# Kernel tuning notes

Hardware: AMD Instinct MI355X
Metric: run time of the kernel (lower is better)

The kernel has to match this reference:

```python
import jax, jax.numpy as jnp
import numpy as np

B, TGT, SRC, DIM = 8, 1024, 1024, 1024

def setup_inputs() -> dict:
    key = jax.random.key(0)
    k1, k2, k3, k4, k5 = jax.random.split(key, 5)
    s = 1.0 / np.sqrt(DIM)
    return {
        "input": jax.random.normal(k1, (B, TGT, DIM), dtype=jnp.float32),
        "context": jax.random.normal(k2, (B, SRC, DIM), dtype=jnp.float32),
        "context_lengths": jax.random.randint(k3, (B,), 1, SRC + 1, dtype=jnp.int64 if jax.config.jax_enable_x64 else jnp.int32),
        "W_in": jax.random.normal(k4, (DIM, DIM), dtype=jnp.float32) * s,   # torch Linear weight [out,in]
        "W_out": jax.random.normal(k5, (DIM, 2 * DIM), dtype=jnp.float32) * s,
    }

def reference(input, context, context_lengths, W_in, W_out):
    # GlobalAttention, attn_type='general', include_rnn=True, dropout=0 (identity)
    # score: (W_in @ h_t) . h_s  -> [B, TGT, SRC]
    h_t = jnp.einsum('btd,ed->bte', input, W_in)
    align = jnp.einsum('bte,bse->bts', h_t, context)
    # mask positions >= length with -inf before softmax over source dim
    mask = jnp.arange(align.shape[-1])[None, :] < context_lengths[:, None]  # [B, SRC]
    align = jnp.where(mask[:, None, :], align, -jnp.inf)
    align_vectors = jax.nn.softmax(align, axis=-1)                         # [B, TGT, SRC]
    c = jnp.einsum('bts,bsd->btd', align_vectors, context)                 # context vector
    concat = jnp.concatenate([c, input], axis=-1)                          # [B, TGT, 2*DIM]
    attn_h = jnp.tanh(jnp.einsum('btf,df->btd', concat, W_out))            # linear_out (no bias) + tanh
    return attn_h, align_vectors
```

## Files before the change

kernel.cpp:

```cpp
#include <hip/hip_runtime.h>

typedef __attribute__((ext_vector_type(8))) short short8;
typedef __attribute__((ext_vector_type(4))) float f32x4;

#define DIM  1024
#define BT   8192
#define NBAT 8

__device__ __forceinline__ unsigned short f2bf(float x){
  union { float f; unsigned u; } un; un.f = x;
  unsigned r = un.u + 0x7fffu + ((un.u >> 16) & 1u);
  return (unsigned short)(r >> 16);
}
__device__ __forceinline__ float bf2f(unsigned short h){
  union { unsigned u; float f; } un; un.u = ((unsigned)h) << 16;
  return un.f;
}

__global__ void split_kernel(const float* __restrict__ x,
                             unsigned short* __restrict__ hi,
                             unsigned short* __restrict__ lo,
                             int n4){
  int stride = gridDim.x * blockDim.x;
  for (int i = blockIdx.x * blockDim.x + threadIdx.x; i < n4; i += stride){
    float4 v = ((const float4*)x)[i];
    ushort4 h, l;
    h.x = f2bf(v.x); l.x = f2bf(v.x - bf2f(h.x));
    h.y = f2bf(v.y); l.y = f2bf(v.y - bf2f(h.y));
    h.z = f2bf(v.z); l.z = f2bf(v.z - bf2f(h.z));
    h.w = f2bf(v.w); l.w = f2bf(v.w - bf2f(h.w));
    ((ushort4*)hi)[i] = h;
    ((ushort4*)lo)[i] = l;
  }
}

__global__ void cvt_kernel(const float* __restrict__ x,
                           unsigned short* __restrict__ hi, int n4){
  int stride = gridDim.x * blockDim.x;
  for (int i = blockIdx.x * blockDim.x + threadIdx.x; i < n4; i += stride){
    float4 v = ((const float4*)x)[i];
    ushort4 h;
    h.x = f2bf(v.x); h.y = f2bf(v.y); h.z = f2bf(v.z); h.w = f2bf(v.w);
    ((ushort4*)hi)[i] = h;
  }
}

__global__ void ctx_prep_kernel(const float* __restrict__ ctx,
                                unsigned short* __restrict__ hi,
                                unsigned short* __restrict__ lo,
                                unsigned short* __restrict__ ctxT){
  __shared__ unsigned short t[64][65];
  int bz = blockIdx.z;
  int s0 = blockIdx.x << 6, d0 = blockIdx.y << 6;
  int tx = threadIdx.x, ty = threadIdx.y;
  const size_t base = (((size_t)bz << 10) + s0) * DIM + d0;
  const float* src = ctx + base;
  unsigned short* hrow = hi + base;
  unsigned short* lrow = lo + base;
  #pragma unroll
  for (int i = ty; i < 64; i += 4){
    float v = src[(size_t)i * DIM + tx];
    unsigned short h = f2bf(v);
    hrow[(size_t)i * DIM + tx] = h;
    lrow[(size_t)i * DIM + tx] = f2bf(v - bf2f(h));
    t[i][tx] = h;
  }
  __syncthreads();
  unsigned short* dst = ctxT + (((size_t)bz << 10) + d0) * DIM + s0;
  #pragma unroll
  for (int i = ty; i < 64; i += 4)
    dst[(size_t)i * DIM + tx] = t[tx][i];
}

__global__ __launch_bounds__(256) void softmax_kernel(float* __restrict__ sc,
                                                      unsigned short* __restrict__ Pb,
                                                      const int* __restrict__ lens){
  const int row = blockIdx.x;
  const int len = lens[row >> 10];
  const int tid = threadIdx.x;
  const int lane = tid & 63, wid = tid >> 6;
  float* rp = sc + ((size_t)row << 10);
  const int s0 = tid << 2;
  float4 v;
  if (s0 < len) v = ((const float4*)rp)[tid];
  else          v = (float4){0.f, 0.f, 0.f, 0.f};
  float x0 = (s0 + 0 < len) ? v.x : -INFINITY;
  float x1 = (s0 + 1 < len) ? v.y : -INFINITY;
  float x2 = (s0 + 2 < len) ? v.z : -INFINITY;
  float x3 = (s0 + 3 < len) ? v.w : -INFINITY;
  float wmax = fmaxf(fmaxf(x0, x1), fmaxf(x2, x3));
  #pragma unroll
  for (int o = 32; o > 0; o >>= 1) wmax = fmaxf(wmax, __shfl_xor(wmax, o));
  __shared__ float red[8];
  if (lane == 0) red[wid] = wmax;
  __syncthreads();
  float mx = fmaxf(fmaxf(red[0], red[1]), fmaxf(red[2], red[3]));
  float e0 = (s0 + 0 < len) ? __expf(x0 - mx) : 0.f;
  float e1 = (s0 + 1 < len) ? __expf(x1 - mx) : 0.f;
  float e2 = (s0 + 2 < len) ? __expf(x2 - mx) : 0.f;
  float e3 = (s0 + 3 < len) ? __expf(x3 - mx) : 0.f;
  float ws = e0 + e1 + e2 + e3;
  #pragma unroll
  for (int o = 32; o > 0; o >>= 1) ws += __shfl_xor(ws, o);
  if (lane == 0) red[4 + wid] = ws;
  __syncthreads();
  float inv = 1.f / (red[4] + red[5] + red[6] + red[7]);
  float4 p; p.x = e0 * inv; p.y = e1 * inv; p.z = e2 * inv; p.w = e3 * inv;
  ((float4*)rp)[tid] = p;
  ushort4 pb; pb.x = f2bf(p.x); pb.y = f2bf(p.y); pb.z = f2bf(p.z); pb.w = f2bf(p.w);
  ((ushort4*)(Pb + ((size_t)row << 10)))[tid] = pb;
}

__device__ __forceinline__ int lds_off(int r, int kb){
  return r * 64 + (((kb ^ ((r >> 1) & 3))) << 4);
}

#define TILEA 16384
#define TILEB 8192

__device__ __forceinline__ void gld16(void* lds, const void* g){
  __builtin_amdgcn_global_load_lds(
      (__attribute__((address_space(1))) void*)(g),
      (__attribute__((address_space(3))) void*)(lds), 16, 0, 0);
}

template<int EPI, int NT, int KSPLIT, int SM>
__global__ __launch_bounds__(512, 2) void gemm_pipe_kernel(
    const unsigned short* __restrict__ Ah,  const unsigned short* __restrict__ Al,
    const unsigned short* __restrict__ Ah2, const unsigned short* __restrict__ Al2,
    const unsigned short* __restrict__ Bh,  const unsigned short* __restrict__ Bl,
    int lda, int ldb,
    float* __restrict__ outF, unsigned short* __restrict__ o1,
    unsigned short* __restrict__ o2, int ldo)
{
  constexpr int OFF_AL = TILEA;
  constexpr int OFF_BH = (SM == 0) ? 2 * TILEA : TILEA;
  constexpr int OFF_BL = OFF_BH + TILEB;
  constexpr int BUFSZ_T = (SM == 2) ? (OFF_BH + TILEB) : (OFF_BL + TILEB);

  __shared__ __align__(16) char sm0[BUFSZ_T];
  __shared__ __align__(16) char sm1[BUFSZ_T];
  __shared__ __align__(16) char sm2[BUFSZ_T];

  const int tid  = threadIdx.x;
  const int lane = tid & 63;
  const int w    = tid >> 6;

  int bx = blockIdx.x, by = blockIdx.y;
  {
    int o = bx + (by << 3);
    int xcd = o & 7, j = o >> 3;
    bx = j & 7;
    by = xcd * (gridDim.y >> 3) + (j >> 3);
  }
  const int m0 = by << 8;
  const int n0 = bx << 7;

  const unsigned short* gAh  = Ah  + (size_t)m0 * lda;
  const unsigned short* gAl  = Al  + (size_t)m0 * lda;
  const unsigned short* gAh2 = Ah2 + (size_t)m0 * lda;
  const unsigned short* gAl2 = Al2 + (size_t)m0 * lda;
  const unsigned short* gBh  = Bh  + (size_t)n0 * ldb;
  const unsigned short* gBl  = Bl  + (size_t)n0 * ldb;

  const int rA0 = (w << 5) + (lane >> 2);
  const int rA1 = rA0 + 16;
  const int rB0 = (w << 4) + (lane >> 2);
  const int cA0 = ((lane & 3) ^ ((rA0 >> 1) & 3)) << 3;
  const int cA1 = ((lane & 3) ^ ((rA1 >> 1) & 3)) << 3;
  const int cB0 = ((lane & 3) ^ ((rB0 >> 1) & 3)) << 3;
  const unsigned short* pAh0  = gAh  + (size_t)rA0 * lda + cA0;
  const unsigned short* pAh1  = gAh  + (size_t)rA1 * lda + cA1;
  const unsigned short* pAl0  = gAl  + (size_t)rA0 * lda + cA0;
  const unsigned short* pAl1  = gAl  + (size_t)rA1 * lda + cA1;
  const unsigned short* pAh20 = gAh2 + (size_t)rA0 * lda + cA0;
  const unsigned short* pAh21 = gAh2 + (size_t)rA1 * lda + cA1;
  const unsigned short* pAl20 = gAl2 + (size_t)rA0 * lda + cA0;
  const unsigned short* pAl21 = gAl2 + (size_t)rA1 * lda + cA1;
  const unsigned short* pBh0  = gBh  + (size_t)rB0 * ldb + cB0;
  const unsigned short* pBl0  = gBl  + (size_t)rB0 * ldb + cB0;
  const int dA0 = (w << 5) << 6;
  const int dA1 = dA0 + (16 << 6);
  const int dB0 = (w << 4) << 6;

  f32x4 acc[4][4];
  #pragma unroll
  for (int m = 0; m < 4; m++)
    #pragma unroll
    for (int n = 0; n < 4; n++)
      acc[m][n] = (f32x4){0.f, 0.f, 0.f, 0.f};

  const int wr = (w >> 1) << 6;
  const int wc = (w & 1) << 6;
  const int fr = lane & 15;
  const int kb = lane >> 4;

  short8 ah, al, bh[4], bl[4];

#define STAGE(WR, KS) do { int _k = (KS);                                   \
    const unsigned short *_s0, *_s1;                                        \
    if (KSPLIT < NT * 32 && _k >= KSPLIT){                                  \
      int _q = _k - KSPLIT;                                                 \
      _s0 = pAh20 + _q; _s1 = pAh21 + _q;                                   \
    } else { _s0 = pAh0 + _k; _s1 = pAh1 + _k; }                            \
    gld16(WR + dA0, _s0);                                                   \
    gld16(WR + dA1, _s1);                                                   \
    if constexpr (SM == 0){                                                 \
      const unsigned short *_s2, *_s3;                                      \
      if (KSPLIT < NT * 32 && _k >= KSPLIT){                                \
        int _q = _k - KSPLIT;                                               \
        _s2 = pAl20 + _q; _s3 = pAl21 + _q;                                 \
      } else { _s2 = pAl0 + _k; _s3 = pAl1 + _k; }                          \
      gld16(WR + OFF_AL + dA0, _s2);                                        \
      gld16(WR + OFF_AL + dA1, _s3);                                        \
    }                                                                       \
    gld16(WR + OFF_BH + dB0, pBh0 + _k);                                    \
    if constexpr (SM != 2)                                                  \
      gld16(WR + OFF_BL + dB0, pBl0 + _k);                                  \
  } while(0)

#define READS_B(RD) do {                                                    \
    _Pragma("unroll")                                                       \
    for (int n = 0; n < 4; n++){                                            \
      int off = lds_off(wc + n * 16 + fr, kb);                              \
      bh[n] = *(const short8*)((RD) + OFF_BH + off);                        \
      if constexpr (SM != 2)                                                \
        bl[n] = *(const short8*)((RD) + OFF_BL + off);                      \
    }                                                                       \
  } while(0)

#define READS_A(RD, M) do {                                                 \
    int off = lds_off(wr + (M) * 16 + fr, kb);                              \
    ah = *(const short8*)((RD) + off);                                      \
    if constexpr (SM == 0) al = *(const short8*)((RD) + OFF_AL + off);      \
  } while(0)

#define MFMA_M(M) do {                                                      \
    __builtin_amdgcn_s_setprio(1);                                          \
    _Pragma("unroll")                                                       \
    for (int n = 0; n < 4; n++){                                            \
      acc[M][n] = __builtin_amdgcn_mfma_f32_16x16x32_bf16(ah, bh[n], acc[M][n], 0, 0, 0); \
      if constexpr (SM != 2)                                                \
        acc[M][n] = __builtin_amdgcn_mfma_f32_16x16x32_bf16(ah, bl[n], acc[M][n], 0, 0, 0); \
      if constexpr (SM == 0)                                                \
        acc[M][n] = __builtin_amdgcn_mfma_f32_16x16x32_bf16(al, bh[n], acc[M][n], 0, 0, 0); \
    }                                                                       \
    __builtin_amdgcn_s_setprio(0);                                          \
  } while(0)

#define BAR() do { __builtin_amdgcn_s_barrier();                            \
                   asm volatile("" ::: "memory"); } while(0)
#define LGKM0() asm volatile("s_waitcnt lgkmcnt(0)" ::: "memory")
#define VMCNT_STEP() do {                                                   \
    if constexpr (SM == 0)      asm volatile("s_waitcnt vmcnt(6)" ::: "memory"); \
    else if constexpr (SM == 1) asm volatile("s_waitcnt vmcnt(4)" ::: "memory"); \
    else                        asm volatile("s_waitcnt vmcnt(3)" ::: "memory"); \
  } while(0)

#define STEP(RD, WR, T) do {                                                \
    int _ks = (((T) + 2 < NT) ? (T) + 2 : NT - 1) << 5;   \
    READS_B(RD); READS_A(RD, 0);                                            \
    STAGE(WR, _ks);                                                         \
    BAR(); LGKM0(); MFMA_M(0); BAR();                                       \
    READS_A(RD, 1);                                                        \
    BAR(); LGKM0(); MFMA_M(1); BAR();                                       \
    READS_A(RD, 2);                                                        \
    BAR(); LGKM0(); MFMA_M(2); BAR();                                       \
    READS_A(RD, 3);                                                        \
    BAR(); LGKM0(); MFMA_M(3);                                              \
    VMCNT_STEP();                                                           \
    BAR();                                                                  \
  } while(0)

  STAGE(sm0, 0);
  STAGE(sm1, 32);
  VMCNT_STEP();
  BAR();

  for (int t = 0; t < NT; t += 3){
    STEP(sm0, sm2, t);
    if (t + 1 < NT) STEP(sm1, sm0, t + 1);
    if (t + 2 < NT) STEP(sm2, sm1, t + 2);
  }
#undef STAGE
#undef READS_B
#undef READS_A
#undef MFMA_M
#undef BAR
#undef LGKM0
#undef VMCNT_STEP
#undef STEP

  const int rbase = (lane >> 4) << 2;
  const int cbase = lane & 15;
  #pragma unroll
  for (int m = 0; m < 4; m++){
    #pragma unroll
    for (int n = 0; n < 4; n++){
      f32x4 v = acc[m][n];
      int col = n0 + wc + n * 16 + cbase;
      #pragma unroll
      for (int j = 0; j < 4; j++){
        int row = m0 + wr + m * 16 + rbase + j;
        float val = v[j];
        size_t idx = (size_t)row * ldo + col;
        if (EPI == 0){
          unsigned short h = f2bf(val);
          o1[idx] = h;
          o2[idx] = f2bf(val - bf2f(h));
        } else {
          outF[idx] = tanhf(val);
        }
      }
    }
  }
}

template<bool SPLIT, int EPI>
__global__ __launch_bounds__(256, 2) void gemm_kernel(
    const unsigned short* __restrict__ Ah, const unsigned short* __restrict__ Al,
    const unsigned short* __restrict__ Bh, const unsigned short* __restrict__ Bl,
    int K, int lda, int ldb,
    long long aStride, long long bStride, long long oStride,
    float* __restrict__ outF, unsigned short* __restrict__ o1,
    unsigned short* __restrict__ o2, int ldo,
    const int* __restrict__ lens, int lmode)
{
  constexpr int TILE = 128 * 64;
  __shared__ char smem[(SPLIT ? 4 : 2) * TILE];
  char* sAh = smem;
  char* sBh = smem + TILE;
  char* sAl = smem + (SPLIT ? 2 : 0) * TILE;
  char* sBl = smem + (SPLIT ? 3 : 0) * TILE;

  const int tid  = threadIdx.x;
  const int lane = tid & 63;
  const int wid  = tid >> 6;
  const int z    = blockIdx.z;

  int bx = blockIdx.x, by = blockIdx.y;
  if (gridDim.x == 8 && gridDim.y == 8){
    int o = bx + (by << 3);
    int k = o & 7, j = o >> 3;
    bx = ((k & 3) << 1) | (j & 1);  by = ((k >> 2) << 2) | (j >> 1);
  }
  const int m0 = by * 128;
  const int n0 = bx * 128;

  int Keff = K;
  if (lmode){
    const int len = lens[z];
    if (lmode == 1 && n0 >= len) return;
    if (lmode == 2){
      int kc = (len + 31) & ~31;
      Keff = kc < K ? kc : K;
    }
  }

  const unsigned short* gAh = Ah + (size_t)z * aStride + (size_t)m0 * lda;
  const unsigned short* gBh = Bh + (size_t)z * bStride + (size_t)n0 * ldb;
  const unsigned short* gAl = SPLIT ? (Al + (size_t)z * aStride + (size_t)m0 * lda) : (const unsigned short*)0;
  const unsigned short* gBl = SPLIT ? (Bl + (size_t)z * bStride + (size_t)n0 * ldb) : (const unsigned short*)0;

  f32x4 acc[4][4];
  #pragma unroll
  for (int m = 0; m < 4; m++)
    #pragma unroll
    for (int n = 0; n < 4; n++)
      acc[m][n] = (f32x4){0.f, 0.f, 0.f, 0.f};

  const int wr = (wid >> 1) * 64;
  const int wc = (wid & 1) * 64;
  const int fr = lane & 15;
  const int kb = lane >> 4;

  for (int k0 = 0; k0 < Keff; k0 += 32){
    __syncthreads();
    #pragma unroll
    for (int it = 0; it < 2; ++it){
      int c = tid + it * 256;
      int r = c >> 2, kk = c & 3;
      int lo = lds_off(r, kk);
      size_t ga = (size_t)r * lda + k0 + kk * 8;
      size_t gb = (size_t)r * ldb + k0 + kk * 8;
      *(short8*)(sAh + lo) = *(const short8*)(gAh + ga);
      *(short8*)(sBh + lo) = *(const short8*)(gBh + gb);
      if (SPLIT){
        *(short8*)(sAl + lo) = *(const short8*)(gAl + ga);
        *(short8*)(sBl + lo) = *(const short8*)(gBl + gb);
      }
    }
    __syncthreads();

    short8 ah[4], bh[4], al[4], bl[4];
    #pragma unroll
    for (int m = 0; m < 4; m++){
      int off = lds_off(wr + m * 16 + fr, kb);
      ah[m] = *(const short8*)(sAh + off);
      if (SPLIT) al[m] = *(const short8*)(sAl + off);
    }
    #pragma unroll
    for (int n = 0; n < 4; n++){
      int off = lds_off(wc + n * 16 + fr, kb);
      bh[n] = *(const short8*)(sBh + off);
      if (SPLIT) bl[n] = *(const short8*)(sBl + off);
    }
    #pragma unroll
    for (int m = 0; m < 4; m++)
      #pragma unroll
      for (int n = 0; n < 4; n++){
        acc[m][n] = __builtin_amdgcn_mfma_f32_16x16x32_bf16(ah[m], bh[n], acc[m][n], 0, 0, 0);
        if (SPLIT){
          acc[m][n] = __builtin_amdgcn_mfma_f32_16x16x32_bf16(ah[m], bl[n], acc[m][n], 0, 0, 0);
          acc[m][n] = __builtin_amdgcn_mfma_f32_16x16x32_bf16(al[m], bh[n], acc[m][n], 0, 0, 0);
        }
      }
  }

  const int rbase = (lane >> 4) * 2 * 2;
  const int cbase = lane & 15;
  #pragma unroll
  for (int m = 0; m < 4; m++){
    #pragma unroll
    for (int n = 0; n < 4; n++){
      f32x4 v = acc[m][n];
      int col = n0 + wc + n * 16 + cbase;
      #pragma unroll
      for (int j = 0; j < 4; j++){
        int row = m0 + wr + m * 16 + rbase + j;
        float val = v[j];
        size_t idx = (size_t)row * ldo + col;
        if (EPI == 0){
          unsigned short h = f2bf(val);
          o1[(size_t)z * oStride + idx] = h;
          o2[(size_t)z * oStride + idx] = f2bf(val - bf2f(h));
        } else if (EPI == 1){
          outF[(size_t)z * oStride + idx] = val;
        } else if (EPI == 4){
          o1[(size_t)z * oStride + idx] = f2bf(val);
        } else {
          outF[idx] = tanhf(val);
        }
      }
    }
  }
}

extern "C" void kernel_launch(void* const* d_in, const int* in_sizes, int n_in,
                              void* d_out, int out_size, void* d_ws, size_t ws_size,
                              hipStream_t stream){
  const float* input   = (const float*)d_in[0];
  const float* context = (const float*)d_in[1];
  const int*   lens    = (const int*)d_in[2];
  const float* Win     = (const float*)d_in[3];
  const float* Wout    = (const float*)d_in[4];
  float* attn  = (float*)d_out;
  float* align = attn + (size_t)BT * DIM;

  char* ws = (char*)d_ws;
  size_t off = 0;
  auto alloc = [&](size_t bytes) -> char* {
    char* p = ws + off; off += (bytes + 255) & ~(size_t)255; return p;
  };
  const size_t MTD = (size_t)BT * DIM;
  unsigned short* in_hi = (unsigned short*)alloc(MTD * 2);
  unsigned short* in_lo = (unsigned short*)alloc(MTD * 2);
  unsigned short* cx_hi = (unsigned short*)alloc(MTD * 2);
  unsigned short* cx_lo = (unsigned short*)alloc(MTD * 2);
  unsigned short* wi_hi = (unsigned short*)alloc((size_t)DIM * DIM * 2);
  unsigned short* wi_lo = (unsigned short*)alloc((size_t)DIM * DIM * 2);
  unsigned short* ht_hi = (unsigned short*)alloc(MTD * 2);
  unsigned short* ht_lo = (unsigned short*)alloc(MTD * 2);
  unsigned short* cxT   = (unsigned short*)alloc(MTD * 2);
  unsigned short* c_hi  = (unsigned short*)alloc(MTD * 2);
  unsigned short* wo_hi = (unsigned short*)alloc((size_t)DIM * 2 * DIM * 2);
  unsigned short* p_bf  = cx_hi;
  if (off > ws_size) return;

  split_kernel<<<4096, 256, 0, stream>>>(input, in_hi, in_lo, (int)(MTD >> 2));
  split_kernel<<<1024, 256, 0, stream>>>(Win, wi_hi, wi_lo, (DIM * DIM) >> 2);
  cvt_kernel<<<2048, 256, 0, stream>>>(Wout, wo_hi, (DIM * 2 * DIM) >> 2);
  ctx_prep_kernel<<<dim3(16, 16, NBAT), dim3(64, 4), 0, stream>>>(context, cx_hi, cx_lo, cxT);

  gemm_pipe_kernel<0, 32, 1024, 0><<<dim3(8, 32), 512, 0, stream>>>(
      in_hi, in_lo, in_hi, in_lo, wi_hi, wi_lo, DIM, DIM,
      nullptr, ht_hi, ht_lo, DIM);
  gemm_kernel<true, 1><<<dim3(8, 8, NBAT), 256, 0, stream>>>(
      ht_hi, ht_lo, cx_hi, cx_lo, DIM, DIM, DIM,
      (long long)DIM * 1024, (long long)DIM * 1024, (long long)DIM * 1024,
      align, nullptr, nullptr, DIM, lens, 1);
  softmax_kernel<<<BT, 256, 0, stream>>>(align, p_bf, lens);
  gemm_kernel<false, 4><<<dim3(8, 8, NBAT), 256, 0, stream>>>(
      p_bf, nullptr, cxT, nullptr, DIM, DIM, DIM,
      (long long)DIM * 1024, (long long)DIM * 1024, (long long)1024 * 1024,
      nullptr, c_hi, nullptr, DIM, lens, 2);
  gemm_pipe_kernel<3, 64, 1024, 2><<<dim3(8, 32), 512, 0, stream>>>(
      c_hi, c_hi, in_hi, in_hi, wo_hi, wo_hi, DIM, 2 * DIM,
      attn, nullptr, nullptr, DIM);
}
```

Before: 234.1 us.

## Load GEMM B fragments directly from global into registers, bypassing LDS

Adds a BREG template mode to the pipelined GEMM in which each wave loads its B-operand fragments straight from global memory into registers, one k-step ahead, instead of staging them through LDS. This shrinks the LDS footprint, removes B LDS reads and writes, and adjusts the vmcnt waits to match. In exchange it duplicates B global loads across waves that share columns, adds register pressure from the double-buffered fragments, and the loads are waited on by the existing vmcnt accounting, which could be fragile.

```diff
diff --git a/kernel.cpp b/kernel.cpp
--- a/kernel.cpp
+++ b/kernel.cpp
@@ -124,7 +124,7 @@
       (__attribute__((address_space(3))) void*)(lds), 16, 0, 0);
 }
 
-template<int EPI, int NT, int KSPLIT, int SM>
+template<int EPI, int NT, int KSPLIT, int SM, int BREG>
 __global__ __launch_bounds__(512, 2) void gemm_pipe_kernel(
     const unsigned short* __restrict__ Ah,  const unsigned short* __restrict__ Al,
     const unsigned short* __restrict__ Ah2, const unsigned short* __restrict__ Al2,
@@ -136,7 +136,9 @@
   constexpr int OFF_AL = TILEA;
   constexpr int OFF_BH = (SM == 0) ? 2 * TILEA : TILEA;
   constexpr int OFF_BL = OFF_BH + TILEB;
-  constexpr int BUFSZ_T = (SM == 2) ? (OFF_BH + TILEB) : (OFF_BL + TILEB);
+  constexpr int BUFSZ_T =
+      BREG ? ((SM == 0) ? 2 * TILEA : TILEA)
+           : ((SM == 2) ? (OFF_BH + TILEB) : (OFF_BL + TILEB));
 
   __shared__ __align__(16) char sm0[BUFSZ_T];
   __shared__ __align__(16) char sm1[BUFSZ_T];
@@ -162,6 +164,11 @@
   const unsigned short* gAl2 = Al2 + (size_t)m0 * lda;
   const unsigned short* gBh  = Bh  + (size_t)n0 * ldb;
   const unsigned short* gBl  = Bl  + (size_t)n0 * ldb;
+
+  const int wr = (w >> 1) << 6;
+  const int wc = (w & 1) << 6;
+  const int fr = lane & 15;
+  const int kb = lane >> 4;
 
   const int rA0 = (w << 5) + (lane >> 2);
   const int rA1 = rA0 + 16;
@@ -182,6 +189,18 @@
   const int dA0 = (w << 5) << 6;
   const int dA1 = dA0 + (16 << 6);
   const int dB0 = (w << 4) << 6;
+  (void)pBh0; (void)pBl0; (void)dB0;
+
+  const unsigned short* pBfh[4];
+  const unsigned short* pBfl[4];
+  if constexpr (BREG){
+    #pragma unroll
+    for (int n = 0; n < 4; n++){
+      size_t roff = (size_t)(wc + n * 16 + fr) * ldb + kb * 8;
+      pBfh[n] = gBh + roff;
+      pBfl[n] = gBl + roff;
+    }
+  }
 
   f32x4 acc[4][4];
   #pragma unroll
@@ -190,12 +209,7 @@
     for (int n = 0; n < 4; n++)
       acc[m][n] = (f32x4){0.f, 0.f, 0.f, 0.f};
 
-  const int wr = (w >> 1) << 6;
-  const int wc = (w & 1) << 6;
-  const int fr = lane & 15;
-  const int kb = lane >> 4;
-
-  short8 ah, al, bh[4], bl[4];
+  short8 ah, al, bh[4], bl[4], bhn[4], bln[4];
 
 #define STAGE(WR, KS) do { int _k = (KS);                                   \
     const unsigned short *_s0, *_s1;                                        \
@@ -214,9 +228,27 @@
       gld16(WR + OFF_AL + dA0, _s2);                                        \
       gld16(WR + OFF_AL + dA1, _s3);                                        \
     }                                                                       \
-    gld16(WR + OFF_BH + dB0, pBh0 + _k);                                    \
-    if constexpr (SM != 2)                                                  \
-      gld16(WR + OFF_BL + dB0, pBl0 + _k);                                  \
+    if constexpr (!BREG){                                                   \
+      gld16(WR + OFF_BH + dB0, pBh0 + _k);                                  \
+      if constexpr (SM != 2)                                                \
+        gld16(WR + OFF_BL + dB0, pBl0 + _k);                                \
+    }                                                                       \
+  } while(0)
+
+#define LOAD_B_NXT(T1) do { int _kb2 = (T1) << 5;                           \
+    _Pragma("unroll")                                                       \
+    for (int n = 0; n < 4; n++){                                            \
+      bhn[n] = *(const short8*)(pBfh[n] + _kb2);                            \
+      if constexpr (SM != 2) bln[n] = *(const short8*)(pBfl[n] + _kb2);     \
+    }                                                                       \
+  } while(0)
+
+#define COPY_B() do {                                                       \
+    _Pragma("unroll")                                                       \
+    for (int n = 0; n < 4; n++){                                            \
+      bh[n] = bhn[n];                                                       \
+      if constexpr (SM != 2) bl[n] = bln[n];                                \
+    }                                                                       \
   } while(0)
 
 #define READS_B(RD) do {                                                    \
@@ -252,14 +284,23 @@
                    asm volatile("" ::: "memory"); } while(0)
 #define LGKM0() asm volatile("s_waitcnt lgkmcnt(0)" ::: "memory")
 #define VMCNT_STEP() do {                                                   \
-    if constexpr (SM == 0)      asm volatile("s_waitcnt vmcnt(6)" ::: "memory"); \
-    else if constexpr (SM == 1) asm volatile("s_waitcnt vmcnt(4)" ::: "memory"); \
-    else                        asm volatile("s_waitcnt vmcnt(3)" ::: "memory"); \
+    if constexpr (BREG){                                                    \
+      if constexpr (SM == 0) asm volatile("s_waitcnt vmcnt(4)" ::: "memory"); \
+      else                   asm volatile("s_waitcnt vmcnt(2)" ::: "memory"); \
+    } else if constexpr (SM == 0) asm volatile("s_waitcnt vmcnt(6)" ::: "memory"); \
+    else if constexpr (SM == 1)   asm volatile("s_waitcnt vmcnt(4)" ::: "memory"); \
+    else                          asm volatile("s_waitcnt vmcnt(3)" ::: "memory"); \
   } while(0)
 
 #define STEP(RD, WR, T) do {                                                \
     int _ks = (((T) + 2 < NT) ? (T) + 2 : NT - 1) << 5;   \
-    READS_B(RD); READS_A(RD, 0);                                            \
+    if constexpr (BREG){                                                    \
+      COPY_B();                                                             \
+      LOAD_B_NXT((((T) + 1 < NT) ? (T) + 1 : NT - 1));                      \
+    } else {                                                                \
+      READS_B(RD);                                                          \
+    }                                                                       \
+    READS_A(RD, 0);                                                         \
     STAGE(WR, _ks);                                                         \
     BAR(); LGKM0(); MFMA_M(0); BAR();                                       \
     READS_A(RD, 1);                                                        \
@@ -272,10 +313,18 @@
     BAR();                                                                  \
   } while(0)
 
-  STAGE(sm0, 0);
-  STAGE(sm1, 32);
-  VMCNT_STEP();
-  BAR();
+  if constexpr (BREG){
+    STAGE(sm0, 0);
+    LOAD_B_NXT(0);
+    STAGE(sm1, 32);
+    VMCNT_STEP();
+    BAR();
+  } else {
+    STAGE(sm0, 0);
+    STAGE(sm1, 32);
+    VMCNT_STEP();
+    BAR();
+  }
 
   for (int t = 0; t < NT; t += 3){
     STEP(sm0, sm2, t);
@@ -283,6 +332,8 @@
     if (t + 2 < NT) STEP(sm2, sm1, t + 2);
   }
 #undef STAGE
+#undef LOAD_B_NXT
+#undef COPY_B
 #undef READS_B
 #undef READS_A
 #undef MFMA_M
@@ -482,7 +533,7 @@
   cvt_kernel<<<2048, 256, 0, stream>>>(Wout, wo_hi, (DIM * 2 * DIM) >> 2);
   ctx_prep_kernel<<<dim3(16, 16, NBAT), dim3(64, 4), 0, stream>>>(context, cx_hi, cx_lo, cxT);
 
-  gemm_pipe_kernel<0, 32, 1024, 0><<<dim3(8, 32), 512, 0, stream>>>(
+  gemm_pipe_kernel<0, 32, 1024, 0, 1><<<dim3(8, 32), 512, 0, stream>>>(
       in_hi, in_lo, in_hi, in_lo, wi_hi, wi_lo, DIM, DIM,
       nullptr, ht_hi, ht_lo, DIM);
   gemm_kernel<true, 1><<<dim3(8, 8, NBAT), 256, 0, stream>>>(
@@ -494,7 +545,7 @@
       p_bf, nullptr, cxT, nullptr, DIM, DIM, DIM,
       (long long)DIM * 1024, (long long)DIM * 1024, (long long)1024 * 1024,
       nullptr, c_hi, nullptr, DIM, lens, 2);
-  gemm_pipe_kernel<3, 64, 1024, 2><<<dim3(8, 32), 512, 0, stream>>>(
+  gemm_pipe_kernel<3, 64, 1024, 2, 1><<<dim3(8, 32), 512, 0, stream>>>(
       c_hi, c_hi, in_hi, in_hi, wo_hi, wo_hi, DIM, 2 * DIM,
       attn, nullptr, nullptr, DIM);
 }
```

Measured after the change: 331.9 us. 1.42x slower.
